# Kernel tuning notes

Measured on AMD Instinct MI355X. Metric: run time of the kernel, lower is better.

The kernel has to match this reference:

```python
import jax, jax.numpy as jnp
import numpy as np

EMB = 128
B = 1024          # number of graphs (segments)
N = 500000        # total nodes
NEG_SLOPE = 0.01  # torch LeakyReLU default


def leaky_relu(v):
    return jnp.where(v >= 0, v, NEG_SLOPE * v)


def setup_inputs() -> dict:
    key = jax.random.key(0)
    ks = jax.random.split(key, 9)
    xg_old = jax.random.normal(ks[0], (B, EMB), dtype=jnp.float32)
    x = jax.random.normal(ks[1], (N, EMB), dtype=jnp.float32)
    batch = jnp.sort(jax.random.randint(ks[2], (N,), 0, B)).astype(jnp.int64)
    s = 1.0 / np.sqrt(EMB)
    w_mask = jax.random.uniform(ks[3], (EMB, 1), jnp.float32, -s, s)
    b_mask = jax.random.uniform(ks[4], (1,), jnp.float32, -s, s)
    w_feat = jax.random.uniform(ks[5], (EMB, EMB), jnp.float32, -s, s)
    b_feat = jax.random.uniform(ks[6], (EMB,), jnp.float32, -s, s)
    s2 = 1.0 / np.sqrt(2 * EMB)
    w_tr = jax.random.uniform(ks[7], (2 * EMB, EMB), jnp.float32, -s2, s2)
    b_tr = jax.random.uniform(ks[8], (EMB,), jnp.float32, -s2, s2)
    return {"xg_old": xg_old, "x": x, "batch": batch,
            "w_mask": w_mask, "b_mask": b_mask,
            "w_feat": w_feat, "b_feat": b_feat,
            "w_tr": w_tr, "b_tr": b_tr}


def reference(xg_old, x, batch, w_mask, b_mask, w_feat, b_feat, w_tr, b_tr):
    batch = batch.astype(jnp.int32)
    # gate score per node, segment-stable softmax over each graph
    gate = (x @ w_mask + b_mask)[:, 0]                        # [N]
    m = jax.ops.segment_max(gate, batch, num_segments=B)      # [B]
    e = jnp.exp(gate - m[batch])                              # [N]
    denom = jax.ops.segment_sum(e, batch, num_segments=B)     # [B]
    alpha = e / denom[batch]                                  # [N]
    # transformed node features, weighted segment-sum pooling
    feat = leaky_relu(x @ w_feat + b_feat)                    # [N, EMB]
    xg = jax.ops.segment_sum(alpha[:, None] * feat, batch, num_segments=B)  # [B, EMB]
    # concat with old global state, linear + LeakyReLU, residual
    cat = jnp.concatenate([xg, xg_old], axis=1)               # [B, 2*EMB]
    out = leaky_relu(cat @ w_tr + b_tr) + xg_old              # [B, EMB]
    return out
```

## Files before the change

### kernel.cpp

```cpp
#include <hip/hip_runtime.h>

typedef __attribute__((ext_vector_type(8))) short short8;
typedef __attribute__((ext_vector_type(4))) float floatx4;

__device__ __forceinline__ float b2f(unsigned int u) { return __uint_as_float(u << 16); }
__device__ __forceinline__ unsigned short f2b(float f) {
    unsigned int u = __float_as_uint(f);
    return (unsigned short)((u + 0x7fffu + ((u >> 16) & 1u)) >> 16);
}

#define EMB 128
#define NN  500000
#define BB  1024
#define BM  128
#define LDX 136
#define LDO 132

__global__ void kdetect(const unsigned short* __restrict__ xr,
                        const int* __restrict__ braw, int* __restrict__ flags, int N)
{
    if (threadIdx.x == 0) {
        int good = 0;
        for (int i = 0; i < 256; ++i) {
            unsigned short u = xr[i];
            unsigned e = (u >> 7) & 0xffu;
            if ((e >= 100u && e <= 140u) || u == 0) ++good;
        }
        flags[0] = (good < 240) ? 1 : 0;
        flags[1] = (braw[N - 1] == 0 && braw[N - 2] != 0) ? 1 : 0;
    }
}

__global__ __launch_bounds__(256)
void kinit(float* __restrict__ denom, float* __restrict__ xg,
           unsigned short* __restrict__ wT, const void* __restrict__ w_feat_,
           const int* __restrict__ flags)
{
    int i = blockIdx.x * 256 + threadIdx.x;
    if (i < BB) denom[i] = 0.f;
    if (i < BB * EMB) xg[i] = 0.f;
    if (i < EMB * EMB) {
        int n = i >> 7, k = i & 127;
        if (flags[0]) wT[i] = f2b(((const float*)w_feat_)[k * EMB + n]);
        else          wT[i] = ((const unsigned short*)w_feat_)[k * EMB + n];
    }
}

__global__ __launch_bounds__(256, 2)
void kmain(const void* __restrict__ x_, const int* __restrict__ braw,
           const void* __restrict__ wm_, const void* __restrict__ bm_,
           const void* __restrict__ b_feat_, const unsigned short* __restrict__ wT,
           const int* __restrict__ flags, float* __restrict__ denom,
           float* __restrict__ xg, int N)
{
    __shared__ __align__(16) char smem[BM * LDX * 2];
    unsigned short* xs = (unsigned short*)smem;
    float* ob = (float*)smem;
    __shared__ int   sb[BM];
    __shared__ float se[BM];
    __shared__ float sbf[EMB];

    int tid = threadIdx.x;
    int n0 = blockIdx.x * BM;
    bool f32  = flags[0] != 0;
    bool is64 = flags[1] != 0;

    if (tid < BM) {
        int n = n0 + tid;
        int s = -1;
        if (n < N) {
            int v = is64 ? braw[2 * n] : braw[n];
            if (v >= 0 && v < BB) s = v;
        }
        sb[tid] = s;
        sbf[tid] = f32 ? ((const float*)b_feat_)[tid]
                       : b2f((unsigned int)((const unsigned short*)b_feat_)[tid]);
    }

    int kofs = (tid & 15) * 8;
    float wf[8];
    float bm;
    if (f32) {
        const float* wm = (const float*)wm_;
#pragma unroll
        for (int j = 0; j < 8; ++j) wf[j] = wm[kofs + j];
        bm = ((const float*)bm_)[0];
    } else {
        const unsigned short* wm = (const unsigned short*)wm_;
        uint4 wv = *(const uint4*)(wm + kofs);
        wf[0] = b2f(wv.x & 0xffffu); wf[1] = b2f(wv.x >> 16);
        wf[2] = b2f(wv.y & 0xffffu); wf[3] = b2f(wv.y >> 16);
        wf[4] = b2f(wv.z & 0xffffu); wf[5] = b2f(wv.z >> 16);
        wf[6] = b2f(wv.w & 0xffffu); wf[7] = b2f(wv.w >> 16);
        bm = b2f((unsigned int)((const unsigned short*)bm_)[0]);
    }

    if (f32) {
        const float* xf = (const float*)x_;
#pragma unroll
        for (int it = 0; it < 8; ++it) {
            int c = tid + it * 256;
            int row = c >> 4;
            int n = n0 + row;
            uint4 o = make_uint4(0u, 0u, 0u, 0u);
            float p = 0.f;
            if (n < N) {
                const float* ptr = xf + (size_t)n * EMB + kofs;
                float4 a = *(const float4*)ptr, b = *(const float4*)(ptr + 4);
                p = wf[0] * a.x + wf[1] * a.y + wf[2] * a.z + wf[3] * a.w
                  + wf[4] * b.x + wf[5] * b.y + wf[6] * b.z + wf[7] * b.w;
                o.x = (unsigned)f2b(a.x) | ((unsigned)f2b(a.y) << 16);
                o.y = (unsigned)f2b(a.z) | ((unsigned)f2b(a.w) << 16);
                o.z = (unsigned)f2b(b.x) | ((unsigned)f2b(b.y) << 16);
                o.w = (unsigned)f2b(b.z) | ((unsigned)f2b(b.w) << 16);
            }
            p += __shfl_xor(p, 1); p += __shfl_xor(p, 2);
            p += __shfl_xor(p, 4); p += __shfl_xor(p, 8);
            if ((tid & 15) == 0) se[row] = p + bm;
            *(uint4*)(xs + row * LDX + kofs) = o;
        }
    } else {
        const unsigned short* xu = (const unsigned short*)x_;
#pragma unroll
        for (int it = 0; it < 8; ++it) {
            int c = tid + it * 256;
            int row = c >> 4;
            int n = n0 + row;
            uint4 v = make_uint4(0u, 0u, 0u, 0u);
            float p = 0.f;
            if (n < N) {
                v = *(const uint4*)(xu + (size_t)n * EMB + kofs);
                p = wf[0] * b2f(v.x & 0xffffu) + wf[1] * b2f(v.x >> 16)
                  + wf[2] * b2f(v.y & 0xffffu) + wf[3] * b2f(v.y >> 16)
                  + wf[4] * b2f(v.z & 0xffffu) + wf[5] * b2f(v.z >> 16)
                  + wf[6] * b2f(v.w & 0xffffu) + wf[7] * b2f(v.w >> 16);
            }
            p += __shfl_xor(p, 1); p += __shfl_xor(p, 2);
            p += __shfl_xor(p, 4); p += __shfl_xor(p, 8);
            if ((tid & 15) == 0) se[row] = p + bm;
            *(uint4*)(xs + row * LDX + kofs) = v;
        }
    }
    __syncthreads();

    int wave = tid >> 6, lane = tid & 63;
    int quad = lane >> 4, l16 = lane & 15;

    if (tid < BM) {
        int s = sb[tid];
        float e = (s >= 0) ? __expf(fminf(se[tid], 60.f)) : 0.f;
        float v = e;
#pragma unroll
        for (int o = 1; o < 64; o <<= 1) {
            float u  = __shfl_up(v, o);
            int   su = __shfl_up(s, o);
            if (lane >= o && su == s) v += u;
        }
        int sn = __shfl_down(s, 1);
        if (s >= 0 && (lane == 63 || sn != s)) atomicAdd(&denom[s], v);
        se[tid] = e;
    }

    floatx4 zero = {0.f, 0.f, 0.f, 0.f};
    floatx4 acc[2][8];
#pragma unroll
    for (int rt = 0; rt < 2; ++rt)
#pragma unroll
        for (int ct = 0; ct < 8; ++ct) acc[rt][ct] = zero;

#pragma unroll
    for (int k0 = 0; k0 < EMB; k0 += 32) {
        short8 a0 = *(const short8*)(xs + (wave * 32 + l16) * LDX + k0 + quad * 8);
        short8 a1 = *(const short8*)(xs + (wave * 32 + 16 + l16) * LDX + k0 + quad * 8);
#pragma unroll
        for (int ct = 0; ct < 8; ++ct) {
            short8 bf = *(const short8*)(wT + (ct * 16 + l16) * EMB + k0 + quad * 8);
            acc[0][ct] = __builtin_amdgcn_mfma_f32_16x16x32_bf16(a0, bf, acc[0][ct], 0, 0, 0);
            acc[1][ct] = __builtin_amdgcn_mfma_f32_16x16x32_bf16(a1, bf, acc[1][ct], 0, 0, 0);
        }
    }
    __syncthreads();

#pragma unroll
    for (int chunk = 0; chunk < 2; ++chunk) {
        if ((wave >> 1) == chunk) {
            int wl = wave & 1;
#pragma unroll
            for (int rt = 0; rt < 2; ++rt)
#pragma unroll
                for (int ct = 0; ct < 8; ++ct)
#pragma unroll
                    for (int r = 0; r < 4; ++r) {
                        int lrow = wl * 32 + rt * 16 + quad * 4 + r;
                        int col = ct * 16 + l16;
                        float v = acc[rt][ct][r] + sbf[col];
                        v = v >= 0.f ? v : 0.01f * v;
                        ob[lrow * LDO + col] = v * se[chunk * 64 + lrow];
                    }
        }
        __syncthreads();

        int col = tid & 127, r0 = (tid >> 7) * 32;
        float a = 0.f; int cur = -1;
        for (int r = r0; r < r0 + 32; ++r) {
            int s = sb[chunk * 64 + r];
            if (s != cur) {
                if (cur >= 0) atomicAdd(&xg[cur * EMB + col], a);
                a = 0.f; cur = s;
            }
            if (s >= 0) a += ob[r * LDO + col];
        }
        if (cur >= 0) atomicAdd(&xg[cur * EMB + col], a);
        __syncthreads();
    }
}

__global__ __launch_bounds__(128)
void kfinal(const float* __restrict__ xg, const float* __restrict__ denom,
            const void* __restrict__ xg_old_, const void* __restrict__ w_tr_,
            const void* __restrict__ b_tr_, const int* __restrict__ flags,
            void* __restrict__ out_)
{
    __shared__ float cat[2 * EMB];
    int b = blockIdx.x, j = threadIdx.x;
    bool f32 = flags[0] != 0;

    float d = denom[b];
    float xgv = xg[b * EMB + j];
    xgv = (d > 0.f) ? xgv / d : 0.f;
    if (xgv != xgv) xgv = 700.0f;
    cat[j] = xgv;
    float old = f32 ? ((const float*)xg_old_)[b * EMB + j]
                    : b2f((unsigned int)((const unsigned short*)xg_old_)[b * EMB + j]);
    cat[EMB + j] = old;
    __syncthreads();

    float acc = f32 ? ((const float*)b_tr_)[j]
                    : b2f((unsigned int)((const unsigned short*)b_tr_)[j]);
    if (f32) {
        const float* w = (const float*)w_tr_;
#pragma unroll 8
        for (int i = 0; i < 2 * EMB; ++i) acc = fmaf(cat[i], w[i * EMB + j], acc);
    } else {
        const unsigned short* w = (const unsigned short*)w_tr_;
#pragma unroll 8
        for (int i = 0; i < 2 * EMB; ++i) acc = fmaf(cat[i], b2f((unsigned int)w[i * EMB + j]), acc);
    }
    acc = acc >= 0.f ? acc : 0.01f * acc;
    acc += old;
    if (acc != acc) acc = 300.0f;

    if (f32) ((float*)out_)[b * EMB + j] = acc;
    else     ((unsigned short*)out_)[b * EMB + j] = f2b(acc);
}

extern "C" void kernel_launch(void* const* d_in, const int* in_sizes, int n_in,
                              void* d_out, int out_size, void* d_ws, size_t ws_size,
                              hipStream_t stream) {
    const void* xg_old = d_in[0];
    const void* x      = d_in[1];
    const int*  braw   = (const int*)d_in[2];
    const void* w_mask = d_in[3];
    const void* b_mask = d_in[4];
    const void* w_feat = d_in[5];
    const void* b_feat = d_in[6];
    const void* w_tr   = d_in[7];
    const void* b_tr   = d_in[8];

    const int N = NN;

    char* ws = (char*)d_ws;
    size_t off = 0;
    int*   flags = (int*)(ws + off);   off += 64;
    float* denom = (float*)(ws + off); off += (size_t)BB * 4;
    float* xg    = (float*)(ws + off); off += (size_t)BB * EMB * 4;
    unsigned short* wT = (unsigned short*)(ws + off); off += (size_t)EMB * EMB * 2;

    kdetect<<<1, 64, 0, stream>>>((const unsigned short*)x, braw, flags, N);
    kinit<<<(BB * EMB + 255) / 256, 256, 0, stream>>>(denom, xg, wT, w_feat, flags);
    kmain<<<(N + BM - 1) / BM, 256, 0, stream>>>(x, braw, w_mask, b_mask, b_feat, wT,
                                                 flags, denom, xg, N);
    kfinal<<<BB, 128, 0, stream>>>(xg, denom, xg_old, w_tr, b_tr, flags, d_out);
}
```

Measured before the change: 468.1 us.

## Fold gate projection into MFMA and reduce pooled rows per wave in registers

The gate weight vector is appended as an extra column tile of the transposed feature weights, so the gate score comes out of the MFMA instead of a separate shuffle-reduced dot product. Each wave now owns its own 32-row LDS tile, which removes block-wide barriers and the LDS staging buffer for the output. Pooling is done directly from accumulator registers: cross-lane shuffles handle the common single-segment case, and per-run atomics handle the rest. Launch bounds move to 4 blocks per CU and the detect kernel is parallelised across a wave. The costs are extra MFMA work for the gate column, bf16 rounding of the gate weights, and more atomics in the mixed-segment path.

```diff
diff --git a/kernel.cpp b/kernel.cpp
--- a/kernel.cpp
+++ b/kernel.cpp
@@ -14,18 +14,22 @@
 #define BB  1024
 #define BM  128
 #define LDX 136
-#define LDO 132
+#define WTR 144
 
 __global__ void kdetect(const unsigned short* __restrict__ xr,
                         const int* __restrict__ braw, int* __restrict__ flags, int N)
 {
-    if (threadIdx.x == 0) {
-        int good = 0;
-        for (int i = 0; i < 256; ++i) {
-            unsigned short u = xr[i];
-            unsigned e = (u >> 7) & 0xffu;
-            if ((e >= 100u && e <= 140u) || u == 0) ++good;
-        }
+    int lane = threadIdx.x;
+    int good = 0;
+#pragma unroll
+    for (int j = 0; j < 4; ++j) {
+        unsigned short u = xr[lane * 4 + j];
+        unsigned e = (u >> 7) & 0xffu;
+        if ((e >= 100u && e <= 140u) || u == 0) ++good;
+    }
+#pragma unroll
+    for (int o = 1; o < 64; o <<= 1) good += __shfl_xor(good, o);
+    if (lane == 0) {
         flags[0] = (good < 240) ? 1 : 0;
         flags[1] = (braw[N - 1] == 0 && braw[N - 2] != 0) ? 1 : 0;
     }
@@ -34,184 +38,183 @@
 __global__ __launch_bounds__(256)
 void kinit(float* __restrict__ denom, float* __restrict__ xg,
            unsigned short* __restrict__ wT, const void* __restrict__ w_feat_,
-           const int* __restrict__ flags)
+           const void* __restrict__ w_mask_, const int* __restrict__ flags)
 {
     int i = blockIdx.x * 256 + threadIdx.x;
     if (i < BB) denom[i] = 0.f;
     if (i < BB * EMB) xg[i] = 0.f;
-    if (i < EMB * EMB) {
+    if (i < WTR * EMB) {
         int n = i >> 7, k = i & 127;
-        if (flags[0]) wT[i] = f2b(((const float*)w_feat_)[k * EMB + n]);
-        else          wT[i] = ((const unsigned short*)w_feat_)[k * EMB + n];
-    }
-}
-
-__global__ __launch_bounds__(256, 2)
+        unsigned short v;
+        if (n < 128) v = flags[0] ? f2b(((const float*)w_feat_)[k * EMB + n])
+                                  : ((const unsigned short*)w_feat_)[k * EMB + n];
+        else if (n == 128) v = flags[0] ? f2b(((const float*)w_mask_)[k])
+                                        : ((const unsigned short*)w_mask_)[k];
+        else v = 0;
+        wT[i] = v;
+    }
+}
+
+__global__ __launch_bounds__(256, 4)
 void kmain(const void* __restrict__ x_, const int* __restrict__ braw,
-           const void* __restrict__ wm_, const void* __restrict__ bm_,
-           const void* __restrict__ b_feat_, const unsigned short* __restrict__ wT,
-           const int* __restrict__ flags, float* __restrict__ denom,
-           float* __restrict__ xg, int N)
-{
-    __shared__ __align__(16) char smem[BM * LDX * 2];
-    unsigned short* xs = (unsigned short*)smem;
-    float* ob = (float*)smem;
+           const void* __restrict__ bm_, const void* __restrict__ bf_,
+           const unsigned short* __restrict__ wT, const int* __restrict__ flags,
+           float* __restrict__ denom, float* __restrict__ xg, int N)
+{
+    __shared__ __align__(16) unsigned short xs[4][32 * LDX];
+    __shared__ float se[BM];
     __shared__ int   sb[BM];
-    __shared__ float se[BM];
-    __shared__ float sbf[EMB];
 
     int tid = threadIdx.x;
-    int n0 = blockIdx.x * BM;
+    int wave = tid >> 6, lane = tid & 63;
+    int quad = lane >> 4, l16 = lane & 15;
+    int woff = wave * 32;
+    int n0 = blockIdx.x * BM + woff;
     bool f32  = flags[0] != 0;
     bool is64 = flags[1] != 0;
-
-    if (tid < BM) {
-        int n = n0 + tid;
-        int s = -1;
-        if (n < N) {
-            int v = is64 ? braw[2 * n] : braw[n];
-            if (v >= 0 && v < BB) s = v;
-        }
-        sb[tid] = s;
-        sbf[tid] = f32 ? ((const float*)b_feat_)[tid]
-                       : b2f((unsigned int)((const unsigned short*)b_feat_)[tid]);
-    }
-
-    int kofs = (tid & 15) * 8;
-    float wf[8];
-    float bm;
-    if (f32) {
-        const float* wm = (const float*)wm_;
-#pragma unroll
-        for (int j = 0; j < 8; ++j) wf[j] = wm[kofs + j];
-        bm = ((const float*)bm_)[0];
-    } else {
-        const unsigned short* wm = (const unsigned short*)wm_;
-        uint4 wv = *(const uint4*)(wm + kofs);
-        wf[0] = b2f(wv.x & 0xffffu); wf[1] = b2f(wv.x >> 16);
-        wf[2] = b2f(wv.y & 0xffffu); wf[3] = b2f(wv.y >> 16);
-        wf[4] = b2f(wv.z & 0xffffu); wf[5] = b2f(wv.z >> 16);
-        wf[6] = b2f(wv.w & 0xffffu); wf[7] = b2f(wv.w >> 16);
-        bm = b2f((unsigned int)((const unsigned short*)bm_)[0]);
+    unsigned short* xw = xs[wave];
+
+    if (lane < 32) {
+        int n = n0 + lane; int s = -1;
+        if (n < N) { int v = is64 ? braw[2 * n] : braw[n]; if (v >= 0 && v < BB) s = v; }
+        sb[woff + lane] = s;
     }
 
     if (f32) {
         const float* xf = (const float*)x_;
 #pragma unroll
         for (int it = 0; it < 8; ++it) {
-            int c = tid + it * 256;
-            int row = c >> 4;
+            int c = it * 64 + lane;
+            int row = c >> 4, k8 = (c & 15) * 8;
             int n = n0 + row;
             uint4 o = make_uint4(0u, 0u, 0u, 0u);
-            float p = 0.f;
             if (n < N) {
-                const float* ptr = xf + (size_t)n * EMB + kofs;
-                float4 a = *(const float4*)ptr, b = *(const float4*)(ptr + 4);
-                p = wf[0] * a.x + wf[1] * a.y + wf[2] * a.z + wf[3] * a.w
-                  + wf[4] * b.x + wf[5] * b.y + wf[6] * b.z + wf[7] * b.w;
+                const float* p = xf + (size_t)n * EMB + k8;
+                float4 a = *(const float4*)p, b = *(const float4*)(p + 4);
                 o.x = (unsigned)f2b(a.x) | ((unsigned)f2b(a.y) << 16);
                 o.y = (unsigned)f2b(a.z) | ((unsigned)f2b(a.w) << 16);
                 o.z = (unsigned)f2b(b.x) | ((unsigned)f2b(b.y) << 16);
                 o.w = (unsigned)f2b(b.z) | ((unsigned)f2b(b.w) << 16);
             }
-            p += __shfl_xor(p, 1); p += __shfl_xor(p, 2);
-            p += __shfl_xor(p, 4); p += __shfl_xor(p, 8);
-            if ((tid & 15) == 0) se[row] = p + bm;
-            *(uint4*)(xs + row * LDX + kofs) = o;
+            *(uint4*)(xw + row * LDX + k8) = o;
         }
     } else {
         const unsigned short* xu = (const unsigned short*)x_;
 #pragma unroll
         for (int it = 0; it < 8; ++it) {
-            int c = tid + it * 256;
-            int row = c >> 4;
+            int c = it * 64 + lane;
+            int row = c >> 4, k8 = (c & 15) * 8;
             int n = n0 + row;
             uint4 v = make_uint4(0u, 0u, 0u, 0u);
-            float p = 0.f;
-            if (n < N) {
-                v = *(const uint4*)(xu + (size_t)n * EMB + kofs);
-                p = wf[0] * b2f(v.x & 0xffffu) + wf[1] * b2f(v.x >> 16)
-                  + wf[2] * b2f(v.y & 0xffffu) + wf[3] * b2f(v.y >> 16)
-                  + wf[4] * b2f(v.z & 0xffffu) + wf[5] * b2f(v.z >> 16)
-                  + wf[6] * b2f(v.w & 0xffffu) + wf[7] * b2f(v.w >> 16);
-            }
-            p += __shfl_xor(p, 1); p += __shfl_xor(p, 2);
-            p += __shfl_xor(p, 4); p += __shfl_xor(p, 8);
-            if ((tid & 15) == 0) se[row] = p + bm;
-            *(uint4*)(xs + row * LDX + kofs) = v;
-        }
-    }
-    __syncthreads();
-
-    int wave = tid >> 6, lane = tid & 63;
-    int quad = lane >> 4, l16 = lane & 15;
-
-    if (tid < BM) {
-        int s = sb[tid];
-        float e = (s >= 0) ? __expf(fminf(se[tid], 60.f)) : 0.f;
-        float v = e;
-#pragma unroll
-        for (int o = 1; o < 64; o <<= 1) {
-            float u  = __shfl_up(v, o);
-            int   su = __shfl_up(s, o);
-            if (lane >= o && su == s) v += u;
-        }
-        int sn = __shfl_down(s, 1);
-        if (s >= 0 && (lane == 63 || sn != s)) atomicAdd(&denom[s], v);
-        se[tid] = e;
+            if (n < N) v = *(const uint4*)(xu + (size_t)n * EMB + k8);
+            *(uint4*)(xw + row * LDX + k8) = v;
+        }
     }
 
     floatx4 zero = {0.f, 0.f, 0.f, 0.f};
-    floatx4 acc[2][8];
+    floatx4 acc[2][9];
 #pragma unroll
     for (int rt = 0; rt < 2; ++rt)
 #pragma unroll
-        for (int ct = 0; ct < 8; ++ct) acc[rt][ct] = zero;
+        for (int ct = 0; ct < 9; ++ct) acc[rt][ct] = zero;
 
 #pragma unroll
     for (int k0 = 0; k0 < EMB; k0 += 32) {
-        short8 a0 = *(const short8*)(xs + (wave * 32 + l16) * LDX + k0 + quad * 8);
-        short8 a1 = *(const short8*)(xs + (wave * 32 + 16 + l16) * LDX + k0 + quad * 8);
-#pragma unroll
-        for (int ct = 0; ct < 8; ++ct) {
+        short8 a0 = *(const short8*)(xw + l16 * LDX + k0 + quad * 8);
+        short8 a1 = *(const short8*)(xw + (16 + l16) * LDX + k0 + quad * 8);
+#pragma unroll
+        for (int ct = 0; ct < 9; ++ct) {
             short8 bf = *(const short8*)(wT + (ct * 16 + l16) * EMB + k0 + quad * 8);
             acc[0][ct] = __builtin_amdgcn_mfma_f32_16x16x32_bf16(a0, bf, acc[0][ct], 0, 0, 0);
             acc[1][ct] = __builtin_amdgcn_mfma_f32_16x16x32_bf16(a1, bf, acc[1][ct], 0, 0, 0);
         }
     }
-    __syncthreads();
-
-#pragma unroll
-    for (int chunk = 0; chunk < 2; ++chunk) {
-        if ((wave >> 1) == chunk) {
-            int wl = wave & 1;
-#pragma unroll
-            for (int rt = 0; rt < 2; ++rt)
-#pragma unroll
-                for (int ct = 0; ct < 8; ++ct)
+
+    if (l16 == 0) {
+#pragma unroll
+        for (int rt = 0; rt < 2; ++rt)
+#pragma unroll
+            for (int r = 0; r < 4; ++r)
+                se[woff + rt * 16 + quad * 4 + r] = acc[rt][8][r];
+    }
+
+    float bm = f32 ? ((const float*)bm_)[0]
+                   : b2f((unsigned int)((const unsigned short*)bm_)[0]);
+
+    if (lane < 32) {
+        int sv = sb[woff + lane];
+        float g = se[woff + lane] + bm;
+        float ev = (sv >= 0) ? __expf(fminf(g, 60.f)) : 0.f;
+        se[woff + lane] = ev;
+        float v = ev;
+#pragma unroll
+        for (int o = 1; o < 32; o <<= 1) {
+            float u  = __shfl_up(v, o);
+            int   su = __shfl_up(sv, o);
+            if (lane >= o && su == sv) v += u;
+        }
+        int sn = __shfl_down(sv, 1);
+        if (sv >= 0 && (lane == 31 || sn != sv)) atomicAdd(&denom[sv], v);
+    }
+
+    float bfv[8];
+#pragma unroll
+    for (int ct = 0; ct < 8; ++ct)
+        bfv[ct] = f32 ? ((const float*)bf_)[ct * 16 + l16]
+                      : b2f((unsigned int)((const unsigned short*)bf_)[ct * 16 + l16]);
+
+    float er[2][4]; int sr[2][4];
+#pragma unroll
+    for (int rt = 0; rt < 2; ++rt)
+#pragma unroll
+        for (int r = 0; r < 4; ++r) {
+            int lr = rt * 16 + quad * 4 + r;
+            er[rt][r] = se[woff + lr];
+            sr[rt][r] = sb[woff + lr];
+        }
+
+    int sF = sb[woff], sL = sb[woff + 31];
+    if (sF == sL) {
+        if (sF >= 0) {
+#pragma unroll
+            for (int ct = 0; ct < 8; ++ct) {
+                float p = 0.f;
+#pragma unroll
+                for (int rt = 0; rt < 2; ++rt)
 #pragma unroll
                     for (int r = 0; r < 4; ++r) {
-                        int lrow = wl * 32 + rt * 16 + quad * 4 + r;
-                        int col = ct * 16 + l16;
-                        float v = acc[rt][ct][r] + sbf[col];
+                        float v = acc[rt][ct][r] + bfv[ct];
                         v = v >= 0.f ? v : 0.01f * v;
-                        ob[lrow * LDO + col] = v * se[chunk * 64 + lrow];
+                        p += v * er[rt][r];
                     }
-        }
-        __syncthreads();
-
-        int col = tid & 127, r0 = (tid >> 7) * 32;
-        float a = 0.f; int cur = -1;
-        for (int r = r0; r < r0 + 32; ++r) {
-            int s = sb[chunk * 64 + r];
-            if (s != cur) {
+                p += __shfl_xor(p, 16);
+                p += __shfl_xor(p, 32);
+                if (quad == (ct & 3))
+                    atomicAdd(&xg[sF * EMB + ct * 16 + l16], p);
+            }
+        }
+    } else {
+#pragma unroll
+        for (int ct = 0; ct < 8; ++ct) {
+            int col = ct * 16 + l16;
+#pragma unroll
+            for (int rt = 0; rt < 2; ++rt) {
+                float a = 0.f; int cur = -1;
+#pragma unroll
+                for (int r = 0; r < 4; ++r) {
+                    int s = sr[rt][r];
+                    float v = acc[rt][ct][r] + bfv[ct];
+                    v = v >= 0.f ? v : 0.01f * v;
+                    v *= er[rt][r];
+                    if (s != cur) {
+                        if (cur >= 0) atomicAdd(&xg[cur * EMB + col], a);
+                        a = 0.f; cur = s;
+                    }
+                    if (s >= 0) a += v;
+                }
                 if (cur >= 0) atomicAdd(&xg[cur * EMB + col], a);
-                a = 0.f; cur = s;
             }
-            if (s >= 0) a += ob[r * LDO + col];
-        }
-        if (cur >= 0) atomicAdd(&xg[cur * EMB + col], a);
-        __syncthreads();
+        }
     }
 }
 
@@ -274,11 +277,11 @@
     int*   flags = (int*)(ws + off);   off += 64;
     float* denom = (float*)(ws + off); off += (size_t)BB * 4;
     float* xg    = (float*)(ws + off); off += (size_t)BB * EMB * 4;
-    unsigned short* wT = (unsigned short*)(ws + off); off += (size_t)EMB * EMB * 2;
+    unsigned short* wT = (unsigned short*)(ws + off); off += (size_t)WTR * EMB * 2;
 
     kdetect<<<1, 64, 0, stream>>>((const unsigned short*)x, braw, flags, N);
-    kinit<<<(BB * EMB + 255) / 256, 256, 0, stream>>>(denom, xg, wT, w_feat, flags);
-    kmain<<<(N + BM - 1) / BM, 256, 0, stream>>>(x, braw, w_mask, b_mask, b_feat, wT,
+    kinit<<<(BB * EMB + 255) / 256, 256, 0, stream>>>(denom, xg, wT, w_feat, w_mask, flags);
+    kmain<<<(N + BM - 1) / BM, 256, 0, stream>>>(x, braw, b_mask, b_feat, wT,
                                                  flags, denom, xg, N);
     kfinal<<<BB, 128, 0, stream>>>(xg, denom, xg_old, w_tr, b_tr, flags, d_out);
 }
```

New measurement: 438.8 us. -6.3%, faster.
